# Kernel tuning notes

Measured on AMD Instinct MI355X. Metric: run time of the kernel, lower is better.

The kernel has to match this reference:

```python
import jax, jax.numpy as jnp
import numpy as np
import math

NDIM = 1
K = 7            # kernel_size ** ndim
C = 256          # channels
G = C            # depthwise -> groups == channels
GC = 1           # group_channels
HID = 32
OMEGA = 30.0
OFFSET_SCALE = 2.0
MIN_SIGMA, MAX_SIGMA = 0.05, 0.5
INIT_SIGMA = 0.3


def setup_inputs() -> dict:
    key = jax.random.key(0)
    ks = jax.random.split(key, 24)
    B, L = 4, 4096
    init_raw = math.log(math.exp(INIT_SIGMA) - 1.0)
    nrm = jax.random.normal
    d = {
        "x": nrm(ks[0], (B, L, C), jnp.float32),
        "raw_sigma": jnp.full((NDIM,), init_raw, jnp.float32),
        # input/output projections (stored as (in, out): y = x @ W + b)
        "w_in": nrm(ks[1], (C, C)) * (1.0 / np.sqrt(C)),
        "b_in": nrm(ks[2], (C,)) * 0.01,
        "w_out": nrm(ks[3], (C, C)) * (1.0 / np.sqrt(C)),
        "b_out": nrm(ks[4], (C,)) * 0.01,
        # dw_conv: depthwise 3-tap conv (OIH with I=1), then 1x1 conv (in,out)
        "dw1_w": nrm(ks[5], (C, 1, 3)) * (1.0 / np.sqrt(3)),
        "dw1_b": nrm(ks[6], (C,)) * 0.01,
        "dw2_w": nrm(ks[7], (C, C)) * (1.0 / np.sqrt(C)),
        "dw2_b": nrm(ks[8], (C,)) * 0.01,
        # offset / mask nets (zero-init in original; small random to exercise sampling)
        "w_off": nrm(ks[9], (C, G * K * NDIM)) * 0.01,
        "b_off": nrm(ks[10], (G * K * NDIM,)) * 0.01,
        "w_mask": nrm(ks[11], (C, G * K)) * 0.01,
        "b_mask": nrm(ks[12], (G * K,)) * 0.01,
        # kernel net: Linear(1,32), SiLU, Linear(32,32), SiLU, Linear(32,32), SiLU, Linear(32, G*GC)
        "k0_w": nrm(ks[13], (NDIM, HID)) * 1.0,
        "k0_b": nrm(ks[14], (HID,)) * 0.01,
        "k1_w": nrm(ks[15], (HID, HID)) * (1.0 / np.sqrt(HID)),
        "k1_b": nrm(ks[16], (HID,)) * 0.01,
        "k2_w": nrm(ks[17], (HID, HID)) * (1.0 / np.sqrt(HID)),
        "k2_b": nrm(ks[18], (HID,)) * 0.01,
        "k3_w": nrm(ks[19], (HID, G * GC)) * (1.0 / np.sqrt(HID)),
        "k3_b": nrm(ks[20], (G * GC,)) * 0.01,
    }
    return d


def _forward(x, raw_sigma, w_in, b_in, w_out, b_out, dw1_w, dw1_b, dw2_w, dw2_b,
             w_off, b_off, w_mask, b_mask, k0_w, k0_b, k1_w, k1_b, k2_w, k2_b, k3_w, k3_b):
    B, L, Cc = x.shape
    grid = jnp.linspace(-0.5, 0.5, K)[:, None]                       # (K, NDIM)
    ref_off = (jnp.arange(K, dtype=x.dtype) - K // 2)[:, None]        # (K, NDIM)

    sigma = jnp.clip(jax.nn.softplus(raw_sigma), MIN_SIGMA, MAX_SIGMA)

    x_proj = x @ w_in + b_in                                          # (B, L, C)

    # dw_conv: depthwise conv3 -> SiLU -> conv1x1, on (B, C, L)
    xc = jnp.transpose(x, (0, 2, 1))
    h = jax.lax.conv_general_dilated(xc, dw1_w, (1,), ((1, 1),),
                                     dimension_numbers=("NCH", "OIH", "NCH"),
                                     feature_group_count=Cc)
    h = jax.nn.silu(h + dw1_b[None, :, None])
    h = jnp.einsum("bcl,cd->bdl", h, dw2_w) + dw2_b[None, :, None]
    x_dw = jnp.transpose(h, (0, 2, 1))                                # (B, L, C)

    # Gaussian envelope over kernel taps
    d2 = (grid / jnp.clip(sigma, 1e-6, None)[None, :]) ** 2
    env = jnp.exp(-0.5 * d2.sum(-1))                                  # (K,)
    env = env / jnp.maximum(env.sum(), 1e-8)

    # implicit kernel weights from kernel net (SIREN-style input scaling)
    kh = jax.nn.silu(grid * OMEGA @ k0_w + k0_b)
    kh = jax.nn.silu(kh @ k1_w + k1_b)
    kh = jax.nn.silu(kh @ k2_w + k2_b)
    kernel_weights = kh @ k3_w + k3_b                                 # (K, G*GC)

    offsets = jnp.tanh(x_dw @ w_off + b_off).reshape(B, L, G, K, NDIM) * OFFSET_SCALE
    pos = jnp.arange(L, dtype=x.dtype).reshape(1, L, 1, 1, 1)
    abs_pos = pos + ref_off.reshape(1, 1, 1, K, NDIM) + offsets       # (B,L,G,K,1)

    # ---- bilinear (linear, ndim=1) sampling with gather ----
    p = jnp.clip(abs_pos[..., 0], 0.0, L - 1)                         # (B,L,G,K)
    pf = p.astype(jnp.int32)
    pc = jnp.minimum(pf + 1, L - 1)
    wc = (p - pf.astype(p.dtype))[..., None]                          # (B,L,G,K,1)
    wf = 1.0 - wc

    x_t = x_proj.reshape(B, L, G, GC).transpose(0, 2, 1, 3)           # (B,G,L,GC)

    def gather(idx):  # idx (B,L,G,K) int -> (B,L,G,K,GC)
        it = idx.transpose(0, 2, 1, 3).reshape(B, G, L * K, 1)
        g = jnp.take_along_axis(x_t, it, axis=2)
        return g.reshape(B, G, L, K, GC).transpose(0, 2, 1, 3, 4)

    sampled = gather(pf) * wf + gather(pc) * wc                       # (B,L,G,K,GC)

    kw = kernel_weights.reshape(G, GC, K).transpose(0, 2, 1)          # (G,K,GC) (raw reshape as in original)
    sampled = sampled * kw[None, None]

    raw_mask = (x_dw @ w_mask + b_mask).reshape(B, L, G, K) * env.reshape(1, 1, 1, K)
    attn = jax.nn.softmax(raw_mask, axis=-1)

    out = (sampled * attn[..., None]).sum(3).reshape(B, L, Cc)
    out = out @ w_out + b_out

    offset_reg = (offsets ** 2).mean()
    entropy = -(attn * jnp.log(attn + 1e-8)).sum(-1).mean()
    return out, offset_reg, -entropy


def reference(x, raw_sigma, w_in, b_in, w_out, b_out, dw1_w, dw1_b, dw2_w, dw2_b,
              w_off, b_off, w_mask, b_mask, k0_w, k0_b, k1_w, k1_b, k2_w, k2_b, k3_w, k3_b):
    return _forward(x, raw_sigma, w_in, b_in, w_out, b_out, dw1_w, dw1_b, dw2_w, dw2_b,
                    w_off, b_off, w_mask, b_mask, k0_w, k0_b, k1_w, k1_b, k2_w, k2_b, k3_w, k3_b)
```

## Files before the change

kernel.cpp:

```cpp
#include <hip/hip_runtime.h>
#include <hip/hip_bf16.h>
#include <hip/hip_fp16.h>
#include <math.h>

#define BB   4
#define LL   4096
#define CCH  256
#define KK   7
#define HIDN 32
#define MTOT (BB * LL)
#define NOFF (CCH * KK)
#define NP   4096
#define NBLK ((NP / 128) * (MTOT / 128))
#define NDWB 4096
#define NPREPB 672

#define LOG2E  1.4426950408889634f
#define NLOG2E2 (-2.8853900817779268f)
#define LN2    0.6931471805599453f

typedef __attribute__((ext_vector_type(8))) short short8;
typedef __attribute__((ext_vector_type(4))) short short4v;
typedef __attribute__((ext_vector_type(4))) float f32x4;
typedef __attribute__((ext_vector_type(2))) __fp16 fp16x2;
typedef __attribute__((address_space(1))) void gvoid_t;
typedef __attribute__((address_space(3))) void svoid_t;

__device__ __forceinline__ float siluf(float v) { return v / (1.0f + expf(-v)); }
__device__ __forceinline__ float bf2f(ushort u) { unsigned x = (unsigned)u << 16; return __uint_as_float(x); }
__device__ __forceinline__ float h2f(ushort u) { __half_raw hr; hr.x = u; return __half2float(__half(hr)); }
__device__ __forceinline__ float rcpf(float x) { return __builtin_amdgcn_rcpf(x); }
__device__ __forceinline__ unsigned pkh(float a, float b) {
    union { fp16x2 h; unsigned u; } cv;
    cv.h = __builtin_amdgcn_cvt_pkrtz(a, b);
    return cv.u;
}
__device__ __forceinline__ void compute_env(const float* raw_sigma, float* ev) {
    float sp = log1pf(expf(raw_sigma[0]));
    sp = fminf(fmaxf(sp, 0.05f), 0.5f);
    float sg = fmaxf(sp, 1e-6f);
    float ssum = 0.0f;
    for (int k = 0; k < KK; ++k) {
        float gk = -0.5f + (float)k * (1.0f / 6.0f);
        float d = gk / sg;
        ev[k] = expf(-0.5f * d * d);
        ssum += ev[k];
    }
    ssum = fmaxf(ssum, 1e-8f);
    for (int k = 0; k < KK; ++k) ev[k] /= ssum;
}

__global__ __launch_bounds__(256) void pre_kernel(
    const float* __restrict__ x, const float* __restrict__ dw1_w, const float* __restrict__ dw1_b,
    const float* __restrict__ w_in, const float* __restrict__ dw2_w, const float* __restrict__ w_out,
    const float* __restrict__ w_off, const float* __restrict__ w_mask,
    const float* __restrict__ raw_sigma,
    const float* __restrict__ k0w, const float* __restrict__ k0b,
    const float* __restrict__ k1w, const float* __restrict__ k1b,
    const float* __restrict__ k2w, const float* __restrict__ k2b,
    const float* __restrict__ k3w, const float* __restrict__ k3b,
    const float* __restrict__ b_off, const float* __restrict__ b_mask,
    __hip_bfloat16* __restrict__ xbf, __hip_bfloat16* __restrict__ hbf,
    __hip_bfloat16* __restrict__ wtin, __hip_bfloat16* __restrict__ wtdw2,
    __hip_bfloat16* __restrict__ wtout, __hip_bfloat16* __restrict__ wtcomb,
    float* __restrict__ kws2, float* __restrict__ bcomb)
{
    const int bid = blockIdx.x;
    const int tid = threadIdx.x;
    __shared__ float t[64][65];
    __shared__ float envs_sh[8];
    __shared__ float h0[KK][HIDN];
    __shared__ float h1[KK][HIDN];
    __shared__ float h2[KK][HIDN];
    __shared__ float flatw[NOFF];

    if (bid < NDWB) {
        size_t base = ((size_t)bid * 256 + tid) * 4;
        int c = (int)(base & (CCH - 1));
        int l = (int)((base >> 8) & (LL - 1));
        float4 xm = *(const float4*)&x[base];
        float4 xl = make_float4(0.f, 0.f, 0.f, 0.f);
        float4 xr = make_float4(0.f, 0.f, 0.f, 0.f);
        if (l > 0)      xl = *(const float4*)&x[base - CCH];
        if (l < LL - 1) xr = *(const float4*)&x[base + CCH];
        float vm[4] = {xm.x, xm.y, xm.z, xm.w};
        float vl[4] = {xl.x, xl.y, xl.z, xl.w};
        float vr[4] = {xr.x, xr.y, xr.z, xr.w};
        ushort xo[4], ho[4];
        #pragma unroll
        for (int j = 0; j < 4; ++j) {
            int cc = c + j;
            float s = vm[j] * dw1_w[cc * 3 + 1] + vl[j] * dw1_w[cc * 3 + 0]
                    + vr[j] * dw1_w[cc * 3 + 2] + dw1_b[cc];
            __hip_bfloat16 hb = __float2bfloat16(siluf(s));
            __hip_bfloat16 xb = __float2bfloat16(vm[j]);
            ho[j] = *(ushort*)&hb;
            xo[j] = *(ushort*)&xb;
        }
        *(short4v*)&xbf[base] = *(short4v*)xo;
        *(short4v*)&hbf[base] = *(short4v*)ho;
        return;
    }
    if (bid < NDWB + NPREPB) {
        const int task = (bid - NDWB) / 112;
        const int bx = (bid - NDWB) % 112;
        if (task == 5) {
            if (bx >= 64) return;
            unsigned u = bx * 256 + tid;
            unsigned row_sel = u >> 5, chunk = u & 31;
            unsigned g = row_sel >> 1, which = row_sel & 1;
            unsigned row = g * 16 + 7 + which * 8;
            short8 z = {};
            *(short8*)((ushort*)wtcomb + (size_t)row * 256 + chunk * 8) = z;
            return;
        }
        const float* src; __hip_bfloat16* dst; int N; int mode = 0;
        switch (task) {
            case 0: src = w_in;  dst = wtin;  N = 256;  break;
            case 1: src = dw2_w; dst = wtdw2; N = 256;  break;
            case 2: src = w_out; dst = wtout; N = 256;  break;
            case 3: src = w_off;  dst = wtcomb; N = NOFF; mode = 1; break;
            default: src = w_mask; dst = wtcomb; N = NOFF; mode = 2; break;
        }
        int ntiles = 4 * (N / 64);
        if (bx >= ntiles) return;
        if (mode == 2 && tid == 0) compute_env(raw_sigma, envs_sh);
        int tk = (bx & 3) * 64;
        int tn = (bx >> 2) * 64;
        #pragma unroll
        for (int i = 0; i < 16; ++i) {
            int e = i * 256 + tid, kk = e >> 6, nn = e & 63;
            t[kk][nn] = src[(size_t)(tk + kk) * N + tn + nn];
        }
        __syncthreads();
        #pragma unroll
        for (int i = 0; i < 16; ++i) {
            int e = i * 256 + tid, nn = e >> 6, kk = e & 63;
            int c = tn + nn;
            float v = t[kk][nn];
            int cp;
            if (mode == 0) cp = c;
            else {
                int g = c / KK, k = c % KK;
                if (mode == 1) { cp = g * 16 + k;     v *= NLOG2E2; }
                else           { cp = g * 16 + 8 + k; v *= envs_sh[k] * LOG2E; }
            }
            dst[(size_t)cp * 256 + tk + kk] = __float2bfloat16(v);
        }
        return;
    }
    {
        int tt = tid;
        if (tt < KK * HIDN) {
            int k = tt / HIDN, j = tt % HIDN;
            float gk = -0.5f + (float)k * (1.0f / 6.0f);
            float v = gk * 30.0f * k0w[j] + k0b[j];
            h0[k][j] = siluf(v);
        }
        __syncthreads();
        if (tt < KK * HIDN) {
            int k = tt / HIDN, j = tt % HIDN;
            float s = k1b[j];
            #pragma unroll
            for (int i = 0; i < HIDN; ++i) s += h0[k][i] * k1w[i * HIDN + j];
            h1[k][j] = siluf(s);
        }
        __syncthreads();
        if (tt < KK * HIDN) {
            int k = tt / HIDN, j = tt % HIDN;
            float s = k2b[j];
            #pragma unroll
            for (int i = 0; i < HIDN; ++i) s += h1[k][i] * k2w[i * HIDN + j];
            h2[k][j] = siluf(s);
        }
        __syncthreads();
        for (int k = 0; k < KK; ++k) {
            float s = k3b[tt];
            #pragma unroll
            for (int i = 0; i < HIDN; ++i) s += h2[k][i] * k3w[i * CCH + tt];
            flatw[k * CCH + tt] = s;
        }
        if (tt == 0) compute_env(raw_sigma, envs_sh);
        __syncthreads();
        #pragma unroll
        for (int k = 0; k < KK; ++k) kws2[tt * 8 + k] = flatw[tt * KK + k];
        kws2[tt * 8 + 7] = 0.0f;
        #pragma unroll
        for (int k = 0; k < KK; ++k) {
            bcomb[tt * 16 + k]     = b_off[tt * KK + k] * NLOG2E2;
            bcomb[tt * 16 + 8 + k] = b_mask[tt * KK + k] * envs_sh[k] * LOG2E;
        }
        bcomb[tt * 16 + 7]  = 0.0f;
        bcomb[tt * 16 + 15] = 0.0f;
    }
}

template<int OUTBF>
__device__ __forceinline__ void gemm_core(
    const __hip_bfloat16* __restrict__ A, const __hip_bfloat16* __restrict__ Bt,
    const float* __restrict__ bias, void* __restrict__ C, int N, char* lds,
    int bx, int by)
{
    char* As = lds;
    char* Bs = lds + 16384;
    const int tid = threadIdx.x, lane = tid & 63, w = tid >> 6;
    const int wr = w >> 1, wc = w & 1;
    const size_t m0 = (size_t)by * 128, n0 = (size_t)bx * 128;

    const int srow = w * 32 + (lane >> 3);
    const int sgr  = (lane & 7) ^ ((lane >> 3) & 7);
    const __hip_bfloat16* a_src = A  + (m0 + srow) * 256 + sgr * 8;
    const __hip_bfloat16* b_src = Bt + (n0 + srow) * 256 + sgr * 8;
    char* a_dst = As + (w * 32) * 128;
    char* b_dst = Bs + (w * 32) * 128;

    f32x4 acc[4][4] = {};

    for (int kt = 0; kt < 4; ++kt) {
        const int k0 = kt * 64;
        #pragma unroll
        for (int inst = 0; inst < 4; ++inst) {
            __builtin_amdgcn_global_load_lds((gvoid_t*)(a_src + k0 + (size_t)inst * 8 * 256),
                                             (svoid_t*)(a_dst + inst * 1024), 16, 0, 0);
            __builtin_amdgcn_global_load_lds((gvoid_t*)(b_src + k0 + (size_t)inst * 8 * 256),
                                             (svoid_t*)(b_dst + inst * 1024), 16, 0, 0);
        }
        __syncthreads();
        #pragma unroll
        for (int ks = 0; ks < 2; ++ks) {
            short8 a[4], b[4];
            #pragma unroll
            for (int i = 0; i < 4; ++i) {
                int mr = wr * 64 + i * 16 + (lane & 15);
                int gk = ks * 4 + (lane >> 4);
                a[i] = *(const short8*)(As + mr * 128 + ((gk ^ (mr & 7)) << 4));
                int nr = wc * 64 + i * 16 + (lane & 15);
                b[i] = *(const short8*)(Bs + nr * 128 + ((gk ^ (nr & 7)) << 4));
            }
            #pragma unroll
            for (int i = 0; i < 4; ++i)
                #pragma unroll
                for (int j = 0; j < 4; ++j)
                    acc[i][j] = __builtin_amdgcn_mfma_f32_16x16x32_bf16(a[i], b[j], acc[i][j], 0, 0, 0);
        }
        __syncthreads();
    }
    #pragma unroll
    for (int j = 0; j < 4; ++j) {
        int col = (int)n0 + wc * 64 + j * 16 + (lane & 15);
        float bb = bias[col];
        #pragma unroll
        for (int i = 0; i < 4; ++i) {
            size_t row0 = m0 + wr * 64 + i * 16 + ((lane >> 4) << 2);
            f32x4 v = acc[i][j];
            #pragma unroll
            for (int q = 0; q < 4; ++q) {
                float val = v[q] + bb;
                if (OUTBF) ((__hip_bfloat16*)C)[(row0 + q) * N + col] = __float2bfloat16(val);
                else       ((float*)C)[(row0 + q) * N + col] = val;
            }
        }
    }
}

__global__ __launch_bounds__(256) void gemm_dual_k256(
    const __hip_bfloat16* __restrict__ A0, const __hip_bfloat16* __restrict__ Bt0,
    const float* __restrict__ bias0, __hip_bfloat16* __restrict__ C0,
    const __hip_bfloat16* __restrict__ A1, const __hip_bfloat16* __restrict__ Bt1,
    const float* __restrict__ bias1, __hip_bfloat16* __restrict__ C1)
{
    __shared__ __align__(16) char lds[32768];
    if (blockIdx.z == 0) gemm_core<1>(A0, Bt0, bias0, C0, 256, lds, blockIdx.x, blockIdx.y);
    else                 gemm_core<1>(A1, Bt1, bias1, C1, 256, lds, blockIdx.x, blockIdx.y);
}

__global__ __launch_bounds__(256) void gemm_out_k256(
    const __hip_bfloat16* __restrict__ A, const __hip_bfloat16* __restrict__ Bt,
    const float* __restrict__ bias, float* __restrict__ C,
    const float* __restrict__ partials, float* __restrict__ out_tail)
{
    __shared__ __align__(16) char lds[32768];
    if (blockIdx.y == 128) {
        if (blockIdx.x != 0) return;
        __shared__ float redr[256], rede[256];
        int t = threadIdx.x;
        float r = 0.0f, e = 0.0f;
        for (int i = t; i < NBLK; i += 256) {
            r += partials[2 * i];
            e += partials[2 * i + 1];
        }
        redr[t] = r; rede[t] = e;
        __syncthreads();
        for (int s = 128; s > 0; s >>= 1) {
            if (t < s) { redr[t] += redr[t + s]; rede[t] += rede[t + s]; }
            __syncthreads();
        }
        if (t == 0) {
            out_tail[0] = redr[0] / 29360128.0f;
            out_tail[1] = rede[0] / 4194304.0f;
        }
        return;
    }
    gemm_core<0>(A, Bt, bias, C, 256, lds, blockIdx.x, blockIdx.y);
}

__global__ __launch_bounds__(256) void gemm_fused_sample(
    const __hip_bfloat16* __restrict__ A,
    const __hip_bfloat16* __restrict__ Bt,
    const float* __restrict__ bcomb,
    const __hip_bfloat16* __restrict__ xproj,
    const float* __restrict__ kws2,
    __hip_bfloat16* __restrict__ out_pre,
    float* __restrict__ partials)
{
    __shared__ __align__(16) char lds[35072];
    char* As = lds;
    char* Bs = lds + 16384;
    const int tid = threadIdx.x, lane = tid & 63, w = tid >> 6;
    const int wr = w >> 1, wc = w & 1;
    const int flat = blockIdx.y * 32 + blockIdx.x;
    const int wid = ((flat & 7) << 9) | (flat >> 3);
    const int bx = wid & 31, by = wid >> 5;
    const size_t m0 = (size_t)by * 128;
    const int n0 = bx * 128, g0 = bx * 8;
    const int l0 = (int)(m0 & (LL - 1));
    const int bidx = (int)(m0 >> 12);

    if (tid < 140) {
        int rr = min(max(l0 - 5 + tid, 0), LL - 1);
        const ushort* src = (const ushort*)xproj + ((size_t)bidx * LL + rr) * CCH + g0;
        __builtin_amdgcn_global_load_lds((gvoid_t*)src,
            (svoid_t*)(lds + 32768 + (tid >> 6) * 1024), 16, 0, 0);
    }

    const int srow = w * 32 + (lane >> 3);
    const int sgr  = (lane & 7) ^ ((lane >> 3) & 7);
    const __hip_bfloat16* a_src = A  + (m0 + srow) * 256 + sgr * 8;
    const __hip_bfloat16* b_src = Bt + (size_t)(n0 + srow) * 256 + sgr * 8;
    char* a_dst = As + (w * 32) * 128;
    char* b_dst = Bs + (w * 32) * 128;

    f32x4 acc[4][4] = {};

    for (int kt = 0; kt < 4; ++kt) {
        const int k0 = kt * 64;
        #pragma unroll
        for (int inst = 0; inst < 4; ++inst) {
            __builtin_amdgcn_global_load_lds((gvoid_t*)(a_src + k0 + (size_t)inst * 8 * 256),
                                             (svoid_t*)(a_dst + inst * 1024), 16, 0, 0);
            __builtin_amdgcn_global_load_lds((gvoid_t*)(b_src + k0 + (size_t)inst * 8 * 256),
                                             (svoid_t*)(b_dst + inst * 1024), 16, 0, 0);
        }
        __syncthreads();
        #pragma unroll
        for (int ks = 0; ks < 2; ++ks) {
            short8 a[4], b[4];
            #pragma unroll
            for (int i = 0; i < 4; ++i) {
                int mr = wr * 64 + i * 16 + (lane & 15);
                int gk = ks * 4 + (lane >> 4);
                a[i] = *(const short8*)(As + mr * 128 + ((gk ^ (mr & 7)) << 4));
                int nr = wc * 64 + i * 16 + (lane & 15);
                b[i] = *(const short8*)(Bs + nr * 128 + ((gk ^ (nr & 7)) << 4));
            }
            #pragma unroll
            for (int i = 0; i < 4; ++i)
                #pragma unroll
                for (int j = 0; j < 4; ++j)
                    acc[j][i] = __builtin_amdgcn_mfma_f32_16x16x32_bf16(b[j], a[i], acc[j][i], 0, 0, 0);
        }
        __syncthreads();
    }

    {
        const int rl = lane & 15, grp = lane >> 4;
        #pragma unroll
        for (int j = 0; j < 4; ++j) {
            float4 bi = *(const float4*)&bcomb[n0 + wc * 64 + j * 16 + grp * 4];
            const int gran = wc * 8 + j * 2 + (grp >> 1);
            #pragma unroll
            for (int i = 0; i < 4; ++i) {
                f32x4 v = acc[j][i];
                uint2 pk;
                pk.x = pkh(v[0] + bi.x, v[1] + bi.y);
                pk.y = pkh(v[2] + bi.z, v[3] + bi.w);
                int row = wr * 64 + i * 16 + rl;
                int addr = row * 256 + ((gran ^ rl) << 4) + (grp & 1) * 8;
                *(uint2*)(lds + addr) = pk;
            }
        }
    }
    __syncthreads();

    const ushort* XsL = (const ushort*)(lds + 32768);
    const int gg = tid & 7, rb = tid >> 3;
    float kwv[KK];
    {
        const float* kp = &kws2[(size_t)(g0 + gg) * 8];
        float4 ka = *(const float4*)kp;
        float4 kb = *(const float4*)(kp + 4);
        kwv[0] = ka.x; kwv[1] = ka.y; kwv[2] = ka.z; kwv[3] = ka.w;
        kwv[4] = kb.x; kwv[5] = kb.y; kwv[6] = kb.z;
    }
    float reg_acc = 0.0f, ent_acc = 0.0f;
    #pragma unroll
    for (int pp = 0; pp < 4; ++pp) {
        const int r = rb + 32 * pp;
        short8 ca = *(const short8*)(lds + r * 256 + (((2 * gg) ^ (r & 15)) << 4));
        short8 cb = *(const short8*)(lds + r * 256 + (((2 * gg + 1) ^ (r & 15)) << 4));
        float mv[KK];
        float mx = -1e30f;
        #pragma unroll
        for (int k = 0; k < KK; ++k) { mv[k] = h2f((ushort)cb[k]); mx = fmaxf(mx, mv[k]); }
        const int l = l0 + r;
        float es = 0.0f, tacc = 0.0f, o = 0.0f;
        #pragma unroll
        for (int k = 0; k < KK; ++k) {
            float d = mv[k] - mx;
            float e = exp2f(d);
            es += e; tacc += e * d;
            float zp = fminf(fmaxf(h2f((ushort)ca[k]), -80.f), 80.f);
            float ee = exp2f(zp);
            float ov = 2.0f * (1.0f - ee) * rcpf(1.0f + ee);
            reg_acc += ov * ov;
            float p = fminf(fmaxf((float)(l + k - 3) + ov, 0.0f), 4095.0f);
            int pf = (int)p;
            float wcf = p - (float)pf;
            int ix  = pf - (l0 - 5);
            int ixc = min(pf + 1, LL - 1) - (l0 - 5);
            float sv = bf2f(XsL[ix * 8 + gg]) * (1.0f - wcf) + bf2f(XsL[ixc * 8 + gg]) * wcf;
            o += sv * kwv[k] * e;
        }
        float inv = rcpf(es);
        ent_acc += tacc * inv - __log2f(es);
        out_pre[(m0 + r) * CCH + g0 + gg] = __float2bfloat16(o * inv);
    }

    #pragma unroll
    for (int d = 1; d < 64; d <<= 1) {
        reg_acc += __shfl_xor(reg_acc, d);
        ent_acc += __shfl_xor(ent_acc, d);
    }
    __syncthreads();
    float* redv = (float*)lds;
    if (lane == 0) { redv[w] = reg_acc; redv[4 + w] = ent_acc; }
    __syncthreads();
    if (tid == 0) {
        float r2 = redv[0] + redv[1] + redv[2] + redv[3];
        float e2 = redv[4] + redv[5] + redv[6] + redv[7];
        partials[wid * 2]     = r2;
        partials[wid * 2 + 1] = e2 * LN2;
    }
}

extern "C" void kernel_launch(void* const* d_in, const int* in_sizes, int n_in,
                              void* d_out, int out_size, void* d_ws, size_t ws_size,
                              hipStream_t stream)
{
    const float* x         = (const float*)d_in[0];
    const float* raw_sigma = (const float*)d_in[1];
    const float* w_in      = (const float*)d_in[2];
    const float* b_in      = (const float*)d_in[3];
    const float* w_out     = (const float*)d_in[4];
    const float* b_out     = (const float*)d_in[5];
    const float* dw1_w     = (const float*)d_in[6];
    const float* dw1_b     = (const float*)d_in[7];
    const float* dw2_w     = (const float*)d_in[8];
    const float* dw2_b     = (const float*)d_in[9];
    const float* w_off     = (const float*)d_in[10];
    const float* b_off     = (const float*)d_in[11];
    const float* w_mask    = (const float*)d_in[12];
    const float* b_mask    = (const float*)d_in[13];
    const float* k0w       = (const float*)d_in[14];
    const float* k0b       = (const float*)d_in[15];
    const float* k1w       = (const float*)d_in[16];
    const float* k1b       = (const float*)d_in[17];
    const float* k2w       = (const float*)d_in[18];
    const float* k2b       = (const float*)d_in[19];
    const float* k3w       = (const float*)d_in[20];
    const float* k3b       = (const float*)d_in[21];

    char* ws = (char*)d_ws;
    const size_t MB8 = (size_t)8 * 1024 * 1024;
    __hip_bfloat16* xbf    = (__hip_bfloat16*)(ws + 0);
    __hip_bfloat16* hbf    = (__hip_bfloat16*)(ws + MB8);
    __hip_bfloat16* xdwbf  = (__hip_bfloat16*)(ws + 2 * MB8);
    __hip_bfloat16* xprojb = (__hip_bfloat16*)(ws + 3 * MB8);
    char* wbase = ws + 4 * MB8;
    __hip_bfloat16* wtin   = (__hip_bfloat16*)(wbase);
    __hip_bfloat16* wtdw2  = (__hip_bfloat16*)(wbase + 131072);
    __hip_bfloat16* wtout  = (__hip_bfloat16*)(wbase + 262144);
    __hip_bfloat16* wtcomb = (__hip_bfloat16*)(wbase + 393216);
    float* bcomb    = (float*)(wbase + 393216 + 2097152);
    float* kws2     = bcomb + NP;
    float* partials = kws2 + 2048;

    pre_kernel<<<NDWB + NPREPB + 1, 256, 0, stream>>>(
        x, dw1_w, dw1_b, w_in, dw2_w, w_out, w_off, w_mask, raw_sigma,
        k0w, k0b, k1w, k1b, k2w, k2b, k3w, k3b, b_off, b_mask,
        xbf, hbf, wtin, wtdw2, wtout, wtcomb, kws2, bcomb);
    gemm_dual_k256<<<dim3(2, 128, 2), 256, 0, stream>>>(xbf, wtin, b_in, xprojb,
                                                        hbf, wtdw2, dw2_b, xdwbf);
    gemm_fused_sample<<<dim3(NP / 128, MTOT / 128), 256, 0, stream>>>(
        xdwbf, wtcomb, bcomb, xprojb, kws2, hbf, partials);
    gemm_out_k256<<<dim3(2, 129), 256, 0, stream>>>(hbf, wtout, b_out, (float*)d_out,
                                                    partials, (float*)d_out + (size_t)MTOT * CCH);
}
```

Measured before the change: 128.2 us.

## Load GEMM operands directly from global into registers, drop LDS staging

All three GEMM kernels now read A and B fragments for the MFMA straight from global memory into registers. This replaces the global_load_lds staging into swizzled shared memory and removes the per-k-tile barriers and the LDS footprint of the plain GEMMs, which could raise occupancy. The trade-off is that operand reuse across waves must now come from cache, and the per-lane 16-byte row-strided loads may be less coalesced. The sampling epilogue is also trimmed: the lower clamp on the offset logit is gone and the ceil neighbour index is taken as floor+1 from the padded LDS tile without the upper bound clamp. At the sequence end this relies on the padded tile holding the clamped value.

Measured after the change: 205.1 us. 60.0% more time.

```diff
diff --git a/kernel.cpp b/kernel.cpp
--- a/kernel.cpp
+++ b/kernel.cpp
@@ -198,44 +198,26 @@
 template<int OUTBF>
 __device__ __forceinline__ void gemm_core(
     const __hip_bfloat16* __restrict__ A, const __hip_bfloat16* __restrict__ Bt,
-    const float* __restrict__ bias, void* __restrict__ C, int N, char* lds,
-    int bx, int by)
-{
-    char* As = lds;
-    char* Bs = lds + 16384;
+    const float* __restrict__ bias, void* __restrict__ C, int N, int bx, int by)
+{
     const int tid = threadIdx.x, lane = tid & 63, w = tid >> 6;
     const int wr = w >> 1, wc = w & 1;
     const size_t m0 = (size_t)by * 128, n0 = (size_t)bx * 128;
-
-    const int srow = w * 32 + (lane >> 3);
-    const int sgr  = (lane & 7) ^ ((lane >> 3) & 7);
-    const __hip_bfloat16* a_src = A  + (m0 + srow) * 256 + sgr * 8;
-    const __hip_bfloat16* b_src = Bt + (n0 + srow) * 256 + sgr * 8;
-    char* a_dst = As + (w * 32) * 128;
-    char* b_dst = Bs + (w * 32) * 128;
+    const ushort* Ab = (const ushort*)A + m0 * 256;
+    const ushort* Bb = (const ushort*)Bt + n0 * 256;
+    const int rl = lane & 15, gk8 = (lane >> 4) * 8;
 
     f32x4 acc[4][4] = {};
-
+    #pragma unroll
     for (int kt = 0; kt < 4; ++kt) {
-        const int k0 = kt * 64;
-        #pragma unroll
-        for (int inst = 0; inst < 4; ++inst) {
-            __builtin_amdgcn_global_load_lds((gvoid_t*)(a_src + k0 + (size_t)inst * 8 * 256),
-                                             (svoid_t*)(a_dst + inst * 1024), 16, 0, 0);
-            __builtin_amdgcn_global_load_lds((gvoid_t*)(b_src + k0 + (size_t)inst * 8 * 256),
-                                             (svoid_t*)(b_dst + inst * 1024), 16, 0, 0);
-        }
-        __syncthreads();
         #pragma unroll
         for (int ks = 0; ks < 2; ++ks) {
+            const int ko = kt * 64 + ks * 32 + gk8;
             short8 a[4], b[4];
             #pragma unroll
             for (int i = 0; i < 4; ++i) {
-                int mr = wr * 64 + i * 16 + (lane & 15);
-                int gk = ks * 4 + (lane >> 4);
-                a[i] = *(const short8*)(As + mr * 128 + ((gk ^ (mr & 7)) << 4));
-                int nr = wc * 64 + i * 16 + (lane & 15);
-                b[i] = *(const short8*)(Bs + nr * 128 + ((gk ^ (nr & 7)) << 4));
+                a[i] = *(const short8*)(Ab + (wr * 64 + i * 16 + rl) * 256 + ko);
+                b[i] = *(const short8*)(Bb + (wc * 64 + i * 16 + rl) * 256 + ko);
             }
             #pragma unroll
             for (int i = 0; i < 4; ++i)
@@ -243,11 +225,10 @@
                 for (int j = 0; j < 4; ++j)
                     acc[i][j] = __builtin_amdgcn_mfma_f32_16x16x32_bf16(a[i], b[j], acc[i][j], 0, 0, 0);
         }
-        __syncthreads();
     }
     #pragma unroll
     for (int j = 0; j < 4; ++j) {
-        int col = (int)n0 + wc * 64 + j * 16 + (lane & 15);
+        int col = (int)n0 + wc * 64 + j * 16 + rl;
         float bb = bias[col];
         #pragma unroll
         for (int i = 0; i < 4; ++i) {
@@ -269,9 +250,8 @@
     const __hip_bfloat16* __restrict__ A1, const __hip_bfloat16* __restrict__ Bt1,
     const float* __restrict__ bias1, __hip_bfloat16* __restrict__ C1)
 {
-    __shared__ __align__(16) char lds[32768];
-    if (blockIdx.z == 0) gemm_core<1>(A0, Bt0, bias0, C0, 256, lds, blockIdx.x, blockIdx.y);
-    else                 gemm_core<1>(A1, Bt1, bias1, C1, 256, lds, blockIdx.x, blockIdx.y);
+    if (blockIdx.z == 0) gemm_core<1>(A0, Bt0, bias0, C0, 256, blockIdx.x, blockIdx.y);
+    else                 gemm_core<1>(A1, Bt1, bias1, C1, 256, blockIdx.x, blockIdx.y);
 }
 
 __global__ __launch_bounds__(256) void gemm_out_k256(
@@ -279,7 +259,6 @@
     const float* __restrict__ bias, float* __restrict__ C,
     const float* __restrict__ partials, float* __restrict__ out_tail)
 {
-    __shared__ __align__(16) char lds[32768];
     if (blockIdx.y == 128) {
         if (blockIdx.x != 0) return;
         __shared__ float redr[256], rede[256];
@@ -301,7 +280,7 @@
         }
         return;
     }
-    gemm_core<0>(A, Bt, bias, C, 256, lds, blockIdx.x, blockIdx.y);
+    gemm_core<0>(A, Bt, bias, C, 256, blockIdx.x, blockIdx.y);
 }
 
 __global__ __launch_bounds__(256) void gemm_fused_sample(
@@ -314,8 +293,6 @@
     float* __restrict__ partials)
 {
     __shared__ __align__(16) char lds[35072];
-    char* As = lds;
-    char* Bs = lds + 16384;
     const int tid = threadIdx.x, lane = tid & 63, w = tid >> 6;
     const int wr = w >> 1, wc = w & 1;
     const int flat = blockIdx.y * 32 + blockIdx.x;
@@ -333,35 +310,21 @@
             (svoid_t*)(lds + 32768 + (tid >> 6) * 1024), 16, 0, 0);
     }
 
-    const int srow = w * 32 + (lane >> 3);
-    const int sgr  = (lane & 7) ^ ((lane >> 3) & 7);
-    const __hip_bfloat16* a_src = A  + (m0 + srow) * 256 + sgr * 8;
-    const __hip_bfloat16* b_src = Bt + (size_t)(n0 + srow) * 256 + sgr * 8;
-    char* a_dst = As + (w * 32) * 128;
-    char* b_dst = Bs + (w * 32) * 128;
+    const ushort* Ab = (const ushort*)A + m0 * 256;
+    const ushort* Bb = (const ushort*)Bt + (size_t)n0 * 256;
+    const int rl = lane & 15, gk8 = (lane >> 4) * 8;
 
     f32x4 acc[4][4] = {};
-
+    #pragma unroll
     for (int kt = 0; kt < 4; ++kt) {
-        const int k0 = kt * 64;
-        #pragma unroll
-        for (int inst = 0; inst < 4; ++inst) {
-            __builtin_amdgcn_global_load_lds((gvoid_t*)(a_src + k0 + (size_t)inst * 8 * 256),
-                                             (svoid_t*)(a_dst + inst * 1024), 16, 0, 0);
-            __builtin_amdgcn_global_load_lds((gvoid_t*)(b_src + k0 + (size_t)inst * 8 * 256),
-                                             (svoid_t*)(b_dst + inst * 1024), 16, 0, 0);
-        }
-        __syncthreads();
         #pragma unroll
         for (int ks = 0; ks < 2; ++ks) {
+            const int ko = kt * 64 + ks * 32 + gk8;
             short8 a[4], b[4];
             #pragma unroll
             for (int i = 0; i < 4; ++i) {
-                int mr = wr * 64 + i * 16 + (lane & 15);
-                int gk = ks * 4 + (lane >> 4);
-                a[i] = *(const short8*)(As + mr * 128 + ((gk ^ (mr & 7)) << 4));
-                int nr = wc * 64 + i * 16 + (lane & 15);
-                b[i] = *(const short8*)(Bs + nr * 128 + ((gk ^ (nr & 7)) << 4));
+                a[i] = *(const short8*)(Ab + (wr * 64 + i * 16 + rl) * 256 + ko);
+                b[i] = *(const short8*)(Bb + (wc * 64 + i * 16 + rl) * 256 + ko);
             }
             #pragma unroll
             for (int i = 0; i < 4; ++i)
@@ -369,11 +332,10 @@
                 for (int j = 0; j < 4; ++j)
                     acc[j][i] = __builtin_amdgcn_mfma_f32_16x16x32_bf16(b[j], a[i], acc[j][i], 0, 0, 0);
         }
-        __syncthreads();
     }
 
     {
-        const int rl = lane & 15, grp = lane >> 4;
+        const int grp = lane >> 4;
         #pragma unroll
         for (int j = 0; j < 4; ++j) {
             float4 bi = *(const float4*)&bcomb[n0 + wc * 64 + j * 16 + grp * 4];
@@ -419,16 +381,15 @@
             float d = mv[k] - mx;
             float e = exp2f(d);
             es += e; tacc += e * d;
-            float zp = fminf(fmaxf(h2f((ushort)ca[k]), -80.f), 80.f);
+            float zp = fminf(h2f((ushort)ca[k]), 80.f);
             float ee = exp2f(zp);
             float ov = 2.0f * (1.0f - ee) * rcpf(1.0f + ee);
             reg_acc += ov * ov;
             float p = fminf(fmaxf((float)(l + k - 3) + ov, 0.0f), 4095.0f);
             int pf = (int)p;
             float wcf = p - (float)pf;
-            int ix  = pf - (l0 - 5);
-            int ixc = min(pf + 1, LL - 1) - (l0 - 5);
-            float sv = bf2f(XsL[ix * 8 + gg]) * (1.0f - wcf) + bf2f(XsL[ixc * 8 + gg]) * wcf;
+            int ix = pf - (l0 - 5);
+            float sv = bf2f(XsL[ix * 8 + gg]) * (1.0f - wcf) + bf2f(XsL[ix * 8 + 8 + gg]) * wcf;
             o += sv * kwv[k] * e;
         }
         float inv = rcpf(es);
```
